# Optimization experiments

Hardware: AMD Instinct MI355X
Metric: run time of the kernel (lower is better)

## Reference

```python
import jax, jax.numpy as jnp
import numpy as np
from jax import lax

NSAMPLE = 16
NEG_SLOPE = 0.1


def leaky(x):
    return jnp.where(x >= 0, x, NEG_SLOPE * x)


def setup_inputs() -> dict:
    key = jax.random.key(0)
    ks = jax.random.split(key, 8)
    B, N1, N2, D = 4, 4096, 4096, 64
    C_in, C_mid, C_out = D + D + 3, 128, 128  # 131 -> 128 -> 128
    xyz1 = jax.random.normal(ks[0], (B, 3, N1), jnp.float32)
    xyz2 = jax.random.normal(ks[1], (B, 3, N2), jnp.float32)
    points1 = jax.random.normal(ks[2], (B, D, N1), jnp.float32)
    points2 = jax.random.normal(ks[3], (B, D, N2), jnp.float32)
    W1 = jax.random.normal(ks[4], (C_mid, C_in), jnp.float32) * 0.05
    b1 = jnp.zeros((C_mid,), jnp.float32)
    W2 = jax.random.normal(ks[5], (C_out, C_mid), jnp.float32) * 0.05
    b2 = jnp.zeros((C_out,), jnp.float32)
    return {"xyz1": xyz1, "xyz2": xyz2, "points1": points1, "points2": points2,
            "W1": W1, "b1": b1, "W2": W2, "b2": b2}


def reference(xyz1, xyz2, points1, points2, W1, b1, W2, b2):
    B, _, N1 = xyz1.shape
    x1 = jnp.transpose(xyz1, (0, 2, 1))      # [B,N1,3]
    x2 = jnp.transpose(xyz2, (0, 2, 1))      # [B,N2,3]
    p1 = jnp.transpose(points1, (0, 2, 1))   # [B,N1,D1]
    p2 = jnp.transpose(points2, (0, 2, 1))   # [B,N2,D2]

    # knn_point: k smallest squared distances from each x1 point into x2
    d2 = (jnp.sum(x1 * x1, -1)[:, :, None]
          + jnp.sum(x2 * x2, -1)[:, None, :]
          - 2.0 * jnp.einsum('bnc,bmc->bnm', x1, x2))  # [B,N1,N2]
    _, knn_idx = lax.top_k(-d2, NSAMPLE)     # [B,N1,K]

    bidx = jnp.arange(B)[:, None, None]
    neighbor_xyz = x2[bidx, knn_idx]         # [B,N1,K,3]
    direction_xyz = neighbor_xyz - x1[:, :, None, :]
    gp2 = p2[bidx, knn_idx]                  # [B,N1,K,D2]
    gp1 = jnp.broadcast_to(p1[:, :, None, :], (B, N1, NSAMPLE, p1.shape[-1]))
    feat = jnp.concatenate([gp1, gp2, direction_xyz], axis=-1)  # [B,N1,K,131]

    h = leaky(jnp.einsum('oc,bnkc->bnko', W1, feat) + b1)
    h = leaky(jnp.einsum('oc,bnkc->bnko', W2, h) + b2)           # [B,N1,K,C_out]

    dist = jnp.maximum(jnp.linalg.norm(direction_xyz, axis=3), 1e-10)  # [B,N1,K]
    inv = 1.0 / dist
    weights = inv / jnp.sum(inv, axis=2, keepdims=True)          # [B,N1,K]

    cost = jnp.einsum('bnk,bnko->bon', weights, h)               # [B,C_out,N1]
    return cost
```

## Files before the change

### kernel.cpp

```cpp
#include <hip/hip_runtime.h>

typedef unsigned short u16;
typedef unsigned int u32;
typedef unsigned long long u64;
typedef __bf16 bf16x8 __attribute__((ext_vector_type(8)));
typedef float f32x4 __attribute__((ext_vector_type(4)));

#define MFMA16(a, b, c) __builtin_amdgcn_mfma_f32_16x16x32_bf16(a, b, c, 0, 0, 0)

static __device__ __forceinline__ u16 f2bf(float f) {
  union { float f; u32 u; } v; v.f = f;
  u32 u = v.u;
  u32 r = (u + 0x7FFFu + ((u >> 16) & 1u)) >> 16;
  return (u16)r;
}

static __device__ __forceinline__ bf16x8 ld16(const u16* p) {
  return __builtin_bit_cast(bf16x8, *(const uint4*)p);
}

static __device__ __forceinline__ u64 u64min(u64 a, u64 b) { return a < b ? a : b; }

static __device__ __forceinline__ u64 bitonic64(u64 v, int lane) {
#pragma unroll
  for (int k = 2; k <= 64; k <<= 1) {
#pragma unroll
    for (int j = k >> 1; j > 0; j >>= 1) {
      u64 o = __shfl_xor(v, j, 64);
      bool up = ((lane & k) == 0);
      bool lower = ((lane & j) == 0);
      u64 mn = v < o ? v : o;
      u64 mx = v < o ? o : v;
      v = (lower == up) ? mn : mx;
    }
  }
  return v;
}

static __device__ __forceinline__ float bitonic64f(float v, int lane) {
#pragma unroll
  for (int k = 2; k <= 64; k <<= 1) {
#pragma unroll
    for (int j = k >> 1; j > 0; j >>= 1) {
      float o = __shfl_xor(v, j, 64);
      bool up = ((lane & k) == 0);
      bool lower = ((lane & j) == 0);
      float mn = fminf(v, o);
      float mx = fmaxf(v, o);
      v = (lower == up) ? mn : mx;
    }
  }
  return v;
}

static __device__ __forceinline__ u32 fkey(float f) {
  u32 bb = __float_as_uint(f);
  u32 sgn = (u32)((int)bb >> 31);
  return bb ^ (sgn | 0x80000000u);
}

static __device__ __forceinline__ float d2of(float x, float y, float z, float s1,
                                             f32x4 c) {
  float dt = __builtin_fmaf(z, c[2], __builtin_fmaf(y, c[1], __fmul_rn(x, c[0])));
  return __fsub_rn(__fadd_rn(s1, c[3]), __fmul_rn(2.0f, dt));
}

__global__ __launch_bounds__(256) void prep_fused(
    const float* __restrict__ points1, const float* __restrict__ points2,
    const float* __restrict__ W1, const float* __restrict__ W2,
    const float* __restrict__ xyz2,
    u16* __restrict__ p1t, u16* __restrict__ p2t,
    u16* __restrict__ W1b, u16* __restrict__ W2b,
    f32x4* __restrict__ candG) {
  __shared__ __align__(4) u16 tile[64 * 66];
  const int g = blockIdx.x;
  const int t = threadIdx.x;
  if (g < 512) {
    const float* src = (g < 256) ? points1 : points2;
    u16* dst = (g < 256) ? p1t : p2t;
    const int gb = g & 255;
    const int b = gb >> 6;
    const int n0 = (gb & 63) << 6;
    const float* sp = src + ((size_t)b << 18);
#pragma unroll
    for (int i = 0; i < 16; i++) {
      int d = (i << 2) + (t >> 6);
      int n = t & 63;
      tile[n * 66 + d] = f2bf(sp[((size_t)d << 12) + n0 + n]);
    }
    __syncthreads();
    u16* dp = dst + ((size_t)(b * 4096 + n0) << 6);
#pragma unroll
    for (int i = 0; i < 8; i++) {
      int n = (i << 3) + (t >> 5);
      int dp2 = t & 31;
      *(u32*)(dp + n * 64 + (dp2 << 1)) = *(const u32*)(tile + n * 66 + (dp2 << 1));
    }
  } else if (g < 656) {
    int i = (g - 512) * 256 + t;
    if (i < 128 * 160) {
      int r = i / 160, c = i - r * 160;
      W1b[i] = (c < 131) ? f2bf(W1[r * 131 + c]) : (u16)0;
    } else {
      int u = i - 128 * 160;
      W2b[u] = f2bf(W2[u]);
    }
  } else {
    int i = (g - 656) * 256 + t;
    int b = i >> 12, m = i & 4095;
    const float* X2 = xyz2 + b * 12288;
    float x = X2[m], y = X2[4096 + m], z = X2[8192 + m];
    float s2 = __fadd_rn(__fadd_rn(__fmul_rn(x, x), __fmul_rn(y, y)),
                         __fmul_rn(z, z));
    f32x4 pk = {x, y, z, s2};
    candG[i] = pk;
  }
}

__global__ __launch_bounds__(256, 2) void knn_kernel(const float* __restrict__ xyz1,
                                                     const f32x4* __restrict__ candG,
                                                     int* __restrict__ knn) {
  __shared__ __align__(16) f32x4 candL[4096];
  __shared__ u64 surv[4][64];
  __shared__ u32 cnt[4];
  const int t = threadIdx.x;
  const int lane = t & 63;
  const int w = t >> 6;
  const int b = blockIdx.x >> 7;
  const int rbase = (blockIdx.x & 127) << 5;
  const float* X1 = xyz1 + b * 12288;
  const f32x4* CG = candG + b * 4096;

#pragma unroll
  for (int i = 0; i < 16; i++) {
    int m = i * 256 + t;
    candL[m] = CG[m];
  }
  __syncthreads();

#pragma unroll 1
  for (int r = 0; r < 8; r++) {
    const int n = rbase + (w << 3) + r;
    const int row = b * 4096 + n;
    const float x = X1[n], y = X1[4096 + n], z = X1[8192 + n];
    const float s1 = __fadd_rn(__fadd_rn(__fmul_rn(x, x), __fmul_rn(y, y)),
                               __fmul_rn(z, z));

    float keys[64];
    float fm = 3e38f;
#pragma unroll
    for (int j = 0; j < 64; j++) {
      const int m = (j << 6) + lane;
      f32x4 c = candL[m];
      float d = d2of(x, y, z, s1, c);
      keys[j] = d;
      fm = fminf(fm, d);
    }

    float tauf = __shfl(bitonic64f(fm, lane), 15, 64);

    if (lane == 0) cnt[w] = 0;
#pragma unroll
    for (int j = 0; j < 64; j++) {
      if (keys[j] <= tauf) {
        u64 k64 = ((u64)fkey(keys[j]) << 32) | (u32)((j << 6) + lane);
        u32 slot = atomicAdd(&cnt[w], 1u);
        if (slot < 64) surv[w][slot] = k64;
      }
    }
    u32 S = cnt[w];

    if (S <= 64) {
      u64 v = (lane < (int)S) ? surv[w][lane] : ~0ull;
      v = bitonic64(v, lane);
      if (lane < 16) knn[row * 16 + lane] = (int)(v & 0xFFFFFFFFull);
    } else {
      u64 prev = 0;
      for (int rr = 0; rr < 16; rr++) {
        u64 lm = ~0ull;
#pragma unroll
        for (int j = 0; j < 64; j++) {
          u64 k64 = ((u64)fkey(keys[j]) << 32) | (u32)((j << 6) + lane);
          if (k64 > prev && k64 < lm) lm = k64;
        }
        u64 gm = lm;
#pragma unroll
        for (int off = 32; off; off >>= 1) gm = u64min(gm, __shfl_xor(gm, off, 64));
        if (lane == 0) knn[row * 16 + rr] = (int)(gm & 0xFFFFFFFFull);
        prev = gm;
      }
    }
  }
}

__global__ __launch_bounds__(256, 3) void mlp_kernel(
    const float* __restrict__ xyz1, const float* __restrict__ xyz2,
    const u16* __restrict__ p1t, const u16* __restrict__ p2t,
    const int* __restrict__ knn,
    const u16* __restrict__ W1b, const float* __restrict__ b1,
    const u16* __restrict__ W2b, const float* __restrict__ b2,
    float* __restrict__ out) {
  __shared__ __align__(16) u16 F[128 * 168];
  __shared__ __align__(16) float winv[128];
  __shared__ __align__(16) float wnorm[128];
  __shared__ __align__(16) float outbuf[128 * 12];
  const int t = threadIdx.x;
  const int g = blockIdx.x;
  const int b = g >> 9;
  const int rbase = (g & 511) << 3;

  {
    const int m = t >> 1, half = t & 1;
    const int n1 = rbase + (m >> 4);
    const uint4* s1p = (const uint4*)(p1t + ((size_t)(b * 4096 + n1) << 6)) + half * 4;
    uint4* d1p = (uint4*)(F + m * 168) + half * 4;
    d1p[0] = s1p[0]; d1p[1] = s1p[1]; d1p[2] = s1p[2]; d1p[3] = s1p[3];
    const int idx = knn[(((size_t)(b * 4096 + n1)) << 4) + (m & 15)];
    const uint4* s2p = (const uint4*)(p2t + ((size_t)(b * 4096 + idx) << 6)) + half * 4;
    uint4* d2p = (uint4*)(F + m * 168 + 64) + half * 4;
    d2p[0] = s2p[0]; d2p[1] = s2p[1]; d2p[2] = s2p[2]; d2p[3] = s2p[3];
  }
  if (t < 128) {
    const int m = t;
    const int n1 = rbase + (m >> 4);
    const int idx = knn[(((size_t)(b * 4096 + n1)) << 4) + (m & 15)];
    const float* X1 = xyz1 + b * 12288;
    const float* X2 = xyz2 + b * 12288;
    float dx = X2[idx] - X1[n1];
    float dy = X2[4096 + idx] - X1[4096 + n1];
    float dz = X2[8192 + idx] - X1[8192 + n1];
    u32 u0 = (u32)f2bf(dx) | ((u32)f2bf(dy) << 16);
    u32 u1 = (u32)f2bf(dz);
    uint4 pk = make_uint4(u0, u1, 0u, 0u);
    *(uint4*)(F + m * 168 + 128) = pk;
    float d = sqrtf(dx * dx + dy * dy + dz * dz);
    winv[m] = 1.0f / fmaxf(d, 1e-10f);
  } else {
    const int m = t - 128;
    uint4 zz = make_uint4(0u, 0u, 0u, 0u);
    uint4* zp = (uint4*)(F + m * 168 + 136);
    zp[0] = zz; zp[1] = zz; zp[2] = zz; zp[3] = zz;
  }
  __syncthreads();

  if (t < 128) {
    const int r = t >> 4;
    float s = 0.f;
#pragma unroll
    for (int k = 0; k < 16; k++) s += winv[(r << 4) + k];
    wnorm[t] = winv[t] / s;
  }

  const int lane = t & 63;
  const int wid = t >> 6;
  const int l15 = lane & 15;
  const int quad = lane >> 4;
  const int koff = quad << 3;
  const int nbase = wid << 5;

  f32x4 acc[8][2];
  const f32x4 z4 = {0.f, 0.f, 0.f, 0.f};
#pragma unroll
  for (int i = 0; i < 8; i++)
#pragma unroll
    for (int j = 0; j < 2; j++) acc[i][j] = z4;

#pragma unroll
  for (int s = 0; s < 5; s++) {
    bf16x8 bf0 = ld16(W1b + (nbase + l15) * 160 + s * 32 + koff);
    bf16x8 bf1 = ld16(W1b + (nbase + 16 + l15) * 160 + s * 32 + koff);
#pragma unroll
    for (int mt = 0; mt < 8; mt++) {
      bf16x8 a = ld16(F + (mt * 16 + l15) * 168 + s * 32 + koff);
      acc[mt][0] = MFMA16(a, bf0, acc[mt][0]);
      acc[mt][1] = MFMA16(a, bf1, acc[mt][1]);
    }
  }
  __syncthreads();

  {
    const float bv0 = b1[nbase + l15];
    const float bv1 = b1[nbase + 16 + l15];
#pragma unroll
    for (int mt = 0; mt < 8; mt++) {
      u16* hrow = F + (mt * 16 + quad * 4) * 168;
#pragma unroll
      for (int r = 0; r < 4; r++) {
        float zv0 = acc[mt][0][r] + bv0;
        zv0 = (zv0 >= 0.f) ? zv0 : 0.1f * zv0;
        hrow[r * 168 + nbase + l15] = f2bf(zv0);
        float zv1 = acc[mt][1][r] + bv1;
        zv1 = (zv1 >= 0.f) ? zv1 : 0.1f * zv1;
        hrow[r * 168 + nbase + 16 + l15] = f2bf(zv1);
      }
    }
  }
  __syncthreads();

  f32x4 acc2[8][2];
#pragma unroll
  for (int i = 0; i < 8; i++)
#pragma unroll
    for (int j = 0; j < 2; j++) acc2[i][j] = z4;

#pragma unroll
  for (int s = 0; s < 4; s++) {
    bf16x8 bf0 = ld16(W2b + (nbase + l15) * 128 + s * 32 + koff);
    bf16x8 bf1 = ld16(W2b + (nbase + 16 + l15) * 128 + s * 32 + koff);
#pragma unroll
    for (int mt = 0; mt < 8; mt++) {
      bf16x8 a = ld16(F + (mt * 16 + l15) * 168 + s * 32 + koff);
      acc2[mt][0] = MFMA16(a, bf0, acc2[mt][0]);
      acc2[mt][1] = MFMA16(a, bf1, acc2[mt][1]);
    }
  }

  {
    const float bv0 = b2[nbase + l15];
    const float bv1 = b2[nbase + 16 + l15];
#pragma unroll
    for (int mt = 0; mt < 8; mt++) {
      const f32x4 w4 = *(const f32x4*)&wnorm[(mt << 4) + (quad << 2)];
      float p0 = 0.f, p1 = 0.f;
#pragma unroll
      for (int r = 0; r < 4; r++) {
        float zv0 = acc2[mt][0][r] + bv0;
        zv0 = (zv0 >= 0.f) ? zv0 : 0.1f * zv0;
        p0 += zv0 * w4[r];
        float zv1 = acc2[mt][1][r] + bv1;
        zv1 = (zv1 >= 0.f) ? zv1 : 0.1f * zv1;
        p1 += zv1 * w4[r];
      }
      p0 += __shfl_xor(p0, 16); p0 += __shfl_xor(p0, 32);
      p1 += __shfl_xor(p1, 16); p1 += __shfl_xor(p1, 32);
      if (quad == 0) {
        outbuf[(nbase + l15) * 12 + mt] = p0;
        outbuf[(nbase + 16 + l15) * 12 + mt] = p1;
      }
    }
  }
  __syncthreads();
  {
    const int ch = t >> 1, half = t & 1;
    f32x4 v = *(const f32x4*)&outbuf[ch * 12 + (half << 2)];
    float* op = out + (((size_t)(b * 128 + ch)) << 12) + rbase + (half << 2);
    *(f32x4*)op = v;
  }
}

extern "C" void kernel_launch(void* const* d_in, const int* in_sizes, int n_in,
                              void* d_out, int out_size, void* d_ws, size_t ws_size,
                              hipStream_t stream) {
  const float* xyz1 = (const float*)d_in[0];
  const float* xyz2 = (const float*)d_in[1];
  const float* points1 = (const float*)d_in[2];
  const float* points2 = (const float*)d_in[3];
  const float* W1 = (const float*)d_in[4];
  const float* b1 = (const float*)d_in[5];
  const float* W2 = (const float*)d_in[6];
  const float* b2 = (const float*)d_in[7];
  float* out = (float*)d_out;

  char* ws = (char*)d_ws;
  int* knn = (int*)ws;
  u16* p1t = (u16*)(ws + 1048576);
  u16* p2t = (u16*)(ws + 3145728);
  u16* W1b = (u16*)(ws + 5242880);
  u16* W2b = (u16*)(ws + 5283840);
  f32x4* candG = (f32x4*)(ws + 5316608);

  hipLaunchKernelGGL(prep_fused, dim3(720), dim3(256), 0, stream,
                     points1, points2, W1, W2, xyz2, p1t, p2t, W1b, W2b, candG);
  hipLaunchKernelGGL(knn_kernel, dim3(512), dim3(256), 0, stream, xyz1, candG, knn);
  hipLaunchKernelGGL(mlp_kernel, dim3(2048), dim3(256), 0, stream,
                     xyz1, xyz2, p1t, p2t, knn, W1b, b1, W2b, b2, out);
}
```

Measured before the change: 161.6 us.

## Fuse KNN selection and MLP into a single kernel via shared-memory neighbor indices

```diff
diff --git a/kernel.cpp b/kernel.cpp
--- a/kernel.cpp
+++ b/kernel.cpp
@@ -117,17 +117,29 @@
   }
 }
 
-__global__ __launch_bounds__(256, 2) void knn_kernel(const float* __restrict__ xyz1,
-                                                     const f32x4* __restrict__ candG,
-                                                     int* __restrict__ knn) {
-  __shared__ __align__(16) f32x4 candL[4096];
+__global__ __launch_bounds__(256, 2) void knn_mlp_fused(
+    const float* __restrict__ xyz1, const f32x4* __restrict__ candG,
+    const u16* __restrict__ p1t, const u16* __restrict__ p2t,
+    const u16* __restrict__ W1b, const float* __restrict__ b1,
+    const u16* __restrict__ W2b, const float* __restrict__ b2,
+    float* __restrict__ out) {
+  __shared__ __align__(16) char LB[65536];
   __shared__ u64 surv[4][64];
   __shared__ u32 cnt[4];
+  __shared__ int idxB[128];
+  __shared__ float dirB[128][3];
+  __shared__ float winv[128];
+  __shared__ float wnorm[128];
+  f32x4* candL = (f32x4*)LB;
+  u16* F = (u16*)LB;
+  float* outbuf = (float*)(LB + 49152);
+
   const int t = threadIdx.x;
   const int lane = t & 63;
   const int w = t >> 6;
-  const int b = blockIdx.x >> 7;
-  const int rbase = (blockIdx.x & 127) << 5;
+  const int g = blockIdx.x;
+  const int b = g >> 9;
+  const int rbase = (g & 511) << 3;
   const float* X1 = xyz1 + b * 12288;
   const f32x4* CG = candG + b * 4096;
 
@@ -139,9 +151,9 @@
   __syncthreads();
 
 #pragma unroll 1
-  for (int r = 0; r < 8; r++) {
-    const int n = rbase + (w << 3) + r;
-    const int row = b * 4096 + n;
+  for (int r = 0; r < 2; r++) {
+    const int lrow = (w << 1) + r;
+    const int n = rbase + lrow;
     const float x = X1[n], y = X1[4096 + n], z = X1[8192 + n];
     const float s1 = __fadd_rn(__fadd_rn(__fmul_rn(x, x), __fmul_rn(y, y)),
                                __fmul_rn(z, z));
@@ -173,7 +185,7 @@
     if (S <= 64) {
       u64 v = (lane < (int)S) ? surv[w][lane] : ~0ull;
       v = bitonic64(v, lane);
-      if (lane < 16) knn[row * 16 + lane] = (int)(v & 0xFFFFFFFFull);
+      if (lane < 16) idxB[(lrow << 4) + lane] = (int)(v & 0xFFFFFFFFull);
     } else {
       u64 prev = 0;
       for (int rr = 0; rr < 16; rr++) {
@@ -186,28 +198,25 @@
         u64 gm = lm;
 #pragma unroll
         for (int off = 32; off; off >>= 1) gm = u64min(gm, __shfl_xor(gm, off, 64));
-        if (lane == 0) knn[row * 16 + rr] = (int)(gm & 0xFFFFFFFFull);
+        if (lane == 0) idxB[(lrow << 4) + rr] = (int)(gm & 0xFFFFFFFFull);
         prev = gm;
       }
     }
   }
-}
-
-__global__ __launch_bounds__(256, 3) void mlp_kernel(
-    const float* __restrict__ xyz1, const float* __restrict__ xyz2,
-    const u16* __restrict__ p1t, const u16* __restrict__ p2t,
-    const int* __restrict__ knn,
-    const u16* __restrict__ W1b, const float* __restrict__ b1,
-    const u16* __restrict__ W2b, const float* __restrict__ b2,
-    float* __restrict__ out) {
-  __shared__ __align__(16) u16 F[128 * 168];
-  __shared__ __align__(16) float winv[128];
-  __shared__ __align__(16) float wnorm[128];
-  __shared__ __align__(16) float outbuf[128 * 12];
-  const int t = threadIdx.x;
-  const int g = blockIdx.x;
-  const int b = g >> 9;
-  const int rbase = (g & 511) << 3;
+
+  if (lane < 32) {
+    const int mloc = (w << 5) + lane;
+    const int n1 = rbase + (mloc >> 4);
+    const int idx = idxB[mloc];
+    f32x4 c = candL[idx];
+    float dx = c[0] - X1[n1];
+    float dy = c[1] - X1[4096 + n1];
+    float dz = c[2] - X1[8192 + n1];
+    dirB[mloc][0] = dx; dirB[mloc][1] = dy; dirB[mloc][2] = dz;
+    float d = sqrtf(dx * dx + dy * dy + dz * dz);
+    winv[mloc] = 1.0f / fmaxf(d, 1e-10f);
+  }
+  __syncthreads();
 
   {
     const int m = t >> 1, half = t & 1;
@@ -215,34 +224,22 @@
     const uint4* s1p = (const uint4*)(p1t + ((size_t)(b * 4096 + n1) << 6)) + half * 4;
     uint4* d1p = (uint4*)(F + m * 168) + half * 4;
     d1p[0] = s1p[0]; d1p[1] = s1p[1]; d1p[2] = s1p[2]; d1p[3] = s1p[3];
-    const int idx = knn[(((size_t)(b * 4096 + n1)) << 4) + (m & 15)];
+    const int idx = idxB[m];
     const uint4* s2p = (const uint4*)(p2t + ((size_t)(b * 4096 + idx) << 6)) + half * 4;
     uint4* d2p = (uint4*)(F + m * 168 + 64) + half * 4;
     d2p[0] = s2p[0]; d2p[1] = s2p[1]; d2p[2] = s2p[2]; d2p[3] = s2p[3];
   }
   if (t < 128) {
     const int m = t;
-    const int n1 = rbase + (m >> 4);
-    const int idx = knn[(((size_t)(b * 4096 + n1)) << 4) + (m & 15)];
-    const float* X1 = xyz1 + b * 12288;
-    const float* X2 = xyz2 + b * 12288;
-    float dx = X2[idx] - X1[n1];
-    float dy = X2[4096 + idx] - X1[4096 + n1];
-    float dz = X2[8192 + idx] - X1[8192 + n1];
-    u32 u0 = (u32)f2bf(dx) | ((u32)f2bf(dy) << 16);
-    u32 u1 = (u32)f2bf(dz);
-    uint4 pk = make_uint4(u0, u1, 0u, 0u);
-    *(uint4*)(F + m * 168 + 128) = pk;
-    float d = sqrtf(dx * dx + dy * dy + dz * dz);
-    winv[m] = 1.0f / fmaxf(d, 1e-10f);
+    u32 u0 = (u32)f2bf(dirB[m][0]) | ((u32)f2bf(dirB[m][1]) << 16);
+    u32 u1 = (u32)f2bf(dirB[m][2]);
+    *(uint4*)(F + m * 168 + 128) = make_uint4(u0, u1, 0u, 0u);
   } else {
     const int m = t - 128;
     uint4 zz = make_uint4(0u, 0u, 0u, 0u);
     uint4* zp = (uint4*)(F + m * 168 + 136);
     zp[0] = zz; zp[1] = zz; zp[2] = zz; zp[3] = zz;
   }
-  __syncthreads();
-
   if (t < 128) {
     const int r = t >> 4;
     float s = 0.f;
@@ -250,13 +247,12 @@
     for (int k = 0; k < 16; k++) s += winv[(r << 4) + k];
     wnorm[t] = winv[t] / s;
   }
-
-  const int lane = t & 63;
-  const int wid = t >> 6;
+  __syncthreads();
+
   const int l15 = lane & 15;
   const int quad = lane >> 4;
   const int koff = quad << 3;
-  const int nbase = wid << 5;
+  const int nbase = w << 5;
 
   f32x4 acc[8][2];
   const f32x4 z4 = {0.f, 0.f, 0.f, 0.f};
@@ -362,16 +358,14 @@
   float* out = (float*)d_out;
 
   char* ws = (char*)d_ws;
-  int* knn = (int*)ws;
-  u16* p1t = (u16*)(ws + 1048576);
-  u16* p2t = (u16*)(ws + 3145728);
-  u16* W1b = (u16*)(ws + 5242880);
-  u16* W2b = (u16*)(ws + 5283840);
-  f32x4* candG = (f32x4*)(ws + 5316608);
+  u16* p1t = (u16*)ws;
+  u16* p2t = (u16*)(ws + 2097152);
+  u16* W1b = (u16*)(ws + 4194304);
+  u16* W2b = (u16*)(ws + 4235264);
+  f32x4* candG = (f32x4*)(ws + 4268032);
 
   hipLaunchKernelGGL(prep_fused, dim3(720), dim3(256), 0, stream,
                      points1, points2, W1, W2, xyz2, p1t, p2t, W1b, W2b, candG);
-  hipLaunchKernelGGL(knn_kernel, dim3(512), dim3(256), 0, stream, xyz1, candG, knn);
-  hipLaunchKernelGGL(mlp_kernel, dim3(2048), dim3(256), 0, stream,
-                     xyz1, xyz2, p1t, p2t, knn, W1b, b1, W2b, b2, out);
-}
+  hipLaunchKernelGGL(knn_mlp_fused, dim3(2048), dim3(256), 0, stream,
+                     xyz1, candG, p1t, p2t, W1b, b1, W2b, b2, out);
+}
```

Result: no change. 164.2 us (+1.6%).

## Fuse prep kernel into KNN kernel and compute candidates in-block

Applied to the files above, without the earlier changes.

```diff
diff --git a/kernel.cpp b/kernel.cpp
--- a/kernel.cpp
+++ b/kernel.cpp
@@ -65,39 +65,25 @@
   return __fsub_rn(__fadd_rn(s1, c[3]), __fmul_rn(2.0f, dt));
 }
 
-__global__ __launch_bounds__(256) void prep_fused(
+__global__ __launch_bounds__(256, 2) void knn_prep(
+    const float* __restrict__ xyz1, const float* __restrict__ xyz2,
     const float* __restrict__ points1, const float* __restrict__ points2,
     const float* __restrict__ W1, const float* __restrict__ W2,
-    const float* __restrict__ xyz2,
     u16* __restrict__ p1t, u16* __restrict__ p2t,
     u16* __restrict__ W1b, u16* __restrict__ W2b,
-    f32x4* __restrict__ candG) {
-  __shared__ __align__(4) u16 tile[64 * 66];
+    int* __restrict__ knn) {
+  __shared__ __align__(16) char LB[65536];
+  f32x4* candL = (f32x4*)LB;
+  u16* tile = (u16*)LB;
+  __shared__ u64 surv[4][64];
+  __shared__ u32 cnt[4];
+  const int t = threadIdx.x;
+  const int lane = t & 63;
+  const int w = t >> 6;
   const int g = blockIdx.x;
-  const int t = threadIdx.x;
-  if (g < 512) {
-    const float* src = (g < 256) ? points1 : points2;
-    u16* dst = (g < 256) ? p1t : p2t;
-    const int gb = g & 255;
-    const int b = gb >> 6;
-    const int n0 = (gb & 63) << 6;
-    const float* sp = src + ((size_t)b << 18);
-#pragma unroll
-    for (int i = 0; i < 16; i++) {
-      int d = (i << 2) + (t >> 6);
-      int n = t & 63;
-      tile[n * 66 + d] = f2bf(sp[((size_t)d << 12) + n0 + n]);
-    }
-    __syncthreads();
-    u16* dp = dst + ((size_t)(b * 4096 + n0) << 6);
-#pragma unroll
-    for (int i = 0; i < 8; i++) {
-      int n = (i << 3) + (t >> 5);
-      int dp2 = t & 31;
-      *(u32*)(dp + n * 64 + (dp2 << 1)) = *(const u32*)(tile + n * 66 + (dp2 << 1));
-    }
-  } else if (g < 656) {
-    int i = (g - 512) * 256 + t;
+
+  if (g < 144) {
+    int i = g * 256 + t;
     if (i < 128 * 160) {
       int r = i / 160, c = i - r * 160;
       W1b[i] = (c < 131) ? f2bf(W1[r * 131 + c]) : (u16)0;
@@ -105,36 +91,44 @@
       int u = i - 128 * 160;
       W2b[u] = f2bf(W2[u]);
     }
-  } else {
-    int i = (g - 656) * 256 + t;
-    int b = i >> 12, m = i & 4095;
-    const float* X2 = xyz2 + b * 12288;
+  }
+
+  {
+    const float* src = (g < 256) ? points1 : points2;
+    u16* dst = (g < 256) ? p1t : p2t;
+    const int gb = g & 255;
+    const int tb = gb >> 6;
+    const int n0 = (gb & 63) << 6;
+    const float* sp = src + ((size_t)tb << 18);
+#pragma unroll
+    for (int i = 0; i < 16; i++) {
+      int d = (i << 2) + (t >> 6);
+      int n = t & 63;
+      tile[n * 66 + d] = f2bf(sp[((size_t)d << 12) + n0 + n]);
+    }
+    __syncthreads();
+    u16* dp = dst + ((size_t)(tb * 4096 + n0) << 6);
+#pragma unroll
+    for (int i = 0; i < 8; i++) {
+      int n = (i << 3) + (t >> 5);
+      int dp2 = t & 31;
+      *(u32*)(dp + n * 64 + (dp2 << 1)) = *(const u32*)(tile + n * 66 + (dp2 << 1));
+    }
+  }
+  __syncthreads();
+
+  const int b = g >> 7;
+  const int rbase = (g & 127) << 5;
+  const float* X1 = xyz1 + b * 12288;
+  const float* X2 = xyz2 + b * 12288;
+#pragma unroll
+  for (int i = 0; i < 16; i++) {
+    int m = i * 256 + t;
     float x = X2[m], y = X2[4096 + m], z = X2[8192 + m];
     float s2 = __fadd_rn(__fadd_rn(__fmul_rn(x, x), __fmul_rn(y, y)),
                          __fmul_rn(z, z));
     f32x4 pk = {x, y, z, s2};
-    candG[i] = pk;
-  }
-}
-
-__global__ __launch_bounds__(256, 2) void knn_kernel(const float* __restrict__ xyz1,
-                                                     const f32x4* __restrict__ candG,
-                                                     int* __restrict__ knn) {
-  __shared__ __align__(16) f32x4 candL[4096];
-  __shared__ u64 surv[4][64];
-  __shared__ u32 cnt[4];
-  const int t = threadIdx.x;
-  const int lane = t & 63;
-  const int w = t >> 6;
-  const int b = blockIdx.x >> 7;
-  const int rbase = (blockIdx.x & 127) << 5;
-  const float* X1 = xyz1 + b * 12288;
-  const f32x4* CG = candG + b * 4096;
-
-#pragma unroll
-  for (int i = 0; i < 16; i++) {
-    int m = i * 256 + t;
-    candL[m] = CG[m];
+    candL[m] = pk;
   }
   __syncthreads();
 
@@ -367,11 +361,9 @@
   u16* p2t = (u16*)(ws + 3145728);
   u16* W1b = (u16*)(ws + 5242880);
   u16* W2b = (u16*)(ws + 5283840);
-  f32x4* candG = (f32x4*)(ws + 5316608);
-
-  hipLaunchKernelGGL(prep_fused, dim3(720), dim3(256), 0, stream,
-                     points1, points2, W1, W2, xyz2, p1t, p2t, W1b, W2b, candG);
-  hipLaunchKernelGGL(knn_kernel, dim3(512), dim3(256), 0, stream, xyz1, candG, knn);
+
+  hipLaunchKernelGGL(knn_prep, dim3(512), dim3(256), 0, stream,
+                     xyz1, xyz2, points1, points2, W1, W2, p1t, p2t, W1b, W2b, knn);
   hipLaunchKernelGGL(mlp_kernel, dim3(2048), dim3(256), 0, stream,
                      xyz1, xyz2, p1t, p2t, knn, W1b, b1, W2b, b2, out);
 }
```

Result: faster. 157.9 us (median of 2 runs) (-2.3%).
